# Kernel tuning notes

Hardware: AMD Instinct MI355X
Metric: run time of the kernel (lower is better)

## Reference

```python
import jax, jax.numpy as jnp
import numpy as np

G = 8  # number of shuffle groups (init default)
GN_EPS = 1e-5


def setup_inputs() -> dict:
    key = jax.random.key(0)
    ks = jax.random.split(key, 9)
    C = 512
    cg = C // (2 * G)  # 32: per-branch channel width
    N, H, W = 32, 64, 64
    return {
        "x": jax.random.normal(ks[0], (N, C, H, W), dtype=jnp.float32),
        "cweight": 0.1 * jax.random.normal(ks[1], (1, cg, 1, 1), dtype=jnp.float32),
        "cbias": jnp.ones((1, cg, 1, 1), dtype=jnp.float32),
        "conv1_w": 0.1 * jax.random.normal(ks[2], (cg, cg), dtype=jnp.float32),
        "conv1_b": 0.1 * jax.random.normal(ks[3], (cg,), dtype=jnp.float32),
        "gn_g": jnp.ones((cg,), dtype=jnp.float32),
        "gn_b": jnp.zeros((cg,), dtype=jnp.float32),
        "convh_w": 0.1 * jax.random.normal(ks[4], (cg, cg), dtype=jnp.float32),
        "convh_b": 0.1 * jax.random.normal(ks[5], (cg,), dtype=jnp.float32),
        "convw_w": 0.1 * jax.random.normal(ks[6], (cg, cg), dtype=jnp.float32),
        "convw_b": 0.1 * jax.random.normal(ks[7], (cg,), dtype=jnp.float32),
    }


def _conv1x1(w, b, x):
    # x: [b, ci, h, w] -> [b, co, h, w]
    return jnp.einsum('oi,bihw->bohw', w, x) + b[None, :, None, None]


def _h_swish(y):
    return y * jnp.clip(y + 3.0, 0.0, 6.0) / 6.0


def reference(x, cweight, cbias, conv1_w, conv1_b, gn_g, gn_b,
              convh_w, convh_b, convw_w, convw_b):
    n, c, h, w = x.shape
    xg = x.reshape(n * G, c // G, h, w)          # [nG, 64, h, w]
    x0, x1 = jnp.split(xg, 2, axis=1)            # each [nG, 32, h, w]

    # --- channel attention branch ---
    gap = jnp.mean(x0, axis=(2, 3), keepdims=True)
    x_channel = x0 * jax.nn.sigmoid(cweight * gap + cbias)

    # --- spatial/coordinate attention branch ---
    x_h = jnp.mean(x1, axis=3, keepdims=True)                       # [nG,32,h,1]
    x_w = jnp.mean(x1, axis=2, keepdims=True).transpose(0, 1, 3, 2)  # [nG,32,w,1]
    x_s = jnp.mean(x1, axis=(2, 3), keepdims=True)                  # [nG,32,1,1]

    y = jnp.concatenate([x_h, x_w], axis=2)      # [nG,32,h+w,1]
    y = _conv1x1(conv1_w, conv1_b, y)
    # GroupNorm with groups == channels: per-channel instance norm over spatial dims
    mu = jnp.mean(y, axis=(2, 3), keepdims=True)
    var = jnp.var(y, axis=(2, 3), keepdims=True)
    y = (y - mu) * jax.lax.rsqrt(var + GN_EPS)
    y = y * gn_g[None, :, None, None] + gn_b[None, :, None, None]
    y = _h_swish(y)

    xh, xw = y[:, :, :h, :], y[:, :, h:, :]
    xw = xw.transpose(0, 1, 3, 2)                # [nG,32,1,w]
    a_h = _conv1x1(convh_w, convh_b, xh)         # [nG,32,h,1]
    a_w = _conv1x1(convw_w, convw_b, xw)         # [nG,32,1,w]
    a_hws = a_h * a_w * x_s                      # [nG,32,h,w]
    x_spatial = x1 * jax.nn.sigmoid(a_hws)

    out = jnp.concatenate([x_channel, x_spatial], axis=1)  # [nG,64,h,w]
    out = out.reshape(n, c, h, w)
    # channel shuffle with groups=2
    out = out.reshape(n, 2, c // 2, h, w).transpose(0, 2, 1, 3, 4).reshape(n, c, h, w)
    return out
```

## Files before the change

kernel.cpp:

```cpp
#include <hip/hip_runtime.h>
#include <hip/hip_bf16.h>
#include <math.h>


#define HW 4096
#define CG 32
#define NBG 256

__device__ __forceinline__ float sigmoidf_(float t) {
    return 1.0f / (1.0f + __expf(-t));
}

__global__ __launch_bounds__(256) void k_reduce(
    const float* __restrict__ x,
    const float* __restrict__ cweight, const float* __restrict__ cbias,
    float* __restrict__ out,
    float* __restrict__ x_s, float* __restrict__ x_h, float* __restrict__ x_w) {
    int wid = threadIdx.x >> 6;
    int l   = threadIdx.x & 63;
    int gp  = blockIdx.x * 4 + wid;
    int bg  = gp >> 6;
    int ch  = gp & 63;
    int n = bg >> 3, g = bg & 7;
    const float4* plane = (const float4*)(x + (size_t)(n * 512 + g * 64 + ch) * HW);

    __shared__ float part[4][64][17];

    float4 v[16];
#pragma unroll
    for (int i = 0; i < 16; ++i) v[i] = plane[i * 64 + l];

    float cs0 = 0.f, cs1 = 0.f, cs2 = 0.f, cs3 = 0.f;
#pragma unroll
    for (int i = 0; i < 16; ++i) {
        cs0 += v[i].x; cs1 += v[i].y; cs2 += v[i].z; cs3 += v[i].w;
        part[wid][i * 4 + (l >> 4)][l & 15] = (v[i].x + v[i].y) + (v[i].z + v[i].w);
    }
    cs0 += __shfl_xor(cs0, 16); cs0 += __shfl_xor(cs0, 32);
    cs1 += __shfl_xor(cs1, 16); cs1 += __shfl_xor(cs1, 32);
    cs2 += __shfl_xor(cs2, 16); cs2 += __shfl_xor(cs2, 32);
    cs3 += __shfl_xor(cs3, 16); cs3 += __shfl_xor(cs3, 32);
    float tot = (cs0 + cs1) + (cs2 + cs3);
    tot += __shfl_xor(tot, 1);
    tot += __shfl_xor(tot, 2);
    tot += __shfl_xor(tot, 4);
    tot += __shfl_xor(tot, 8);

    __syncthreads();
    float rsum = 0.f;
#pragma unroll
    for (int j = 0; j < 16; ++j) rsum += part[wid][l][j];

    if (ch < CG) {
        float sc = sigmoidf_(cweight[ch] * (tot * (1.0f / HW)) + cbias[ch]);
        int cc = g * 64 + ch;
        int cf = 2 * (cc & 255) + (cc >> 8);
        float4* dst = (float4*)(out + (size_t)(n * 512 + cf) * HW);
#pragma unroll
        for (int i = 0; i < 16; ++i) {
            float4 t = v[i];
            t.x *= sc; t.y *= sc; t.z *= sc; t.w *= sc;
            dst[i * 64 + l] = t;
        }
    } else {
        int c1 = ch - CG;
        if (l == 0) x_s[bg * CG + c1] = tot * (1.0f / HW);
        x_h[(size_t)(bg * CG + c1) * 64 + l] = rsum * (1.0f / 64.0f);
        if (l < 16) {
            float4 cw;
            cw.x = cs0 * (1.0f / 64.0f); cw.y = cs1 * (1.0f / 64.0f);
            cw.z = cs2 * (1.0f / 64.0f); cw.w = cs3 * (1.0f / 64.0f);
            ((float4*)(x_w + (size_t)(bg * CG + c1) * 64))[l] = cw;
        }
    }
}

__global__ __launch_bounds__(128) void k_mid(
    const float* __restrict__ x_h, const float* __restrict__ x_w,
    const float* __restrict__ x_s,
    const float* __restrict__ w1, const float* __restrict__ b1,
    const float* __restrict__ gn_g, const float* __restrict__ gn_b,
    const float* __restrict__ wh, const float* __restrict__ bh,
    const float* __restrict__ ww, const float* __restrict__ bw,
    float* __restrict__ a_h, float* __restrict__ a_ws) {
    int bg = blockIdx.x;
    int t  = threadIdx.x;

    __shared__ float sy[32][129];
    __shared__ float spart[2][4][32];
    __shared__ float sscale[32], sshift[32];

    float vloc[32];
#pragma unroll
    for (int i = 0; i < 32; ++i) {
        vloc[i] = (t < 64) ? x_h[(size_t)(bg * CG + i) * 64 + t]
                           : x_w[(size_t)(bg * CG + i) * 64 + (t - 64)];
    }

    for (int o = 0; o < 32; ++o) {
        float acc = b1[o];
#pragma unroll
        for (int i = 0; i < 32; ++i) acc += w1[o * 32 + i] * vloc[i];
        sy[o][t] = acc;
    }
    __syncthreads();

    {
        int o = t & 31, seg = t >> 5;
        float s = 0.f, ss = 0.f;
#pragma unroll
        for (int p = 0; p < 32; ++p) {
            float v = sy[o][seg * 32 + p];
            s += v; ss += v * v;
        }
        spart[0][seg][o] = s; spart[1][seg][o] = ss;
    }
    __syncthreads();
    if (t < 32) {
        float s  = spart[0][0][t] + spart[0][1][t] + spart[0][2][t] + spart[0][3][t];
        float ss = spart[1][0][t] + spart[1][1][t] + spart[1][2][t] + spart[1][3][t];
        float mu = s * (1.0f / 128.0f);
        float var = ss * (1.0f / 128.0f) - mu * mu;
        float rstd = rsqrtf(var + 1e-5f);
        float sc = rstd * gn_g[t];
        sscale[t] = sc;
        sshift[t] = gn_b[t] - mu * sc;
    }
    __syncthreads();

    float z[32];
#pragma unroll
    for (int i = 0; i < 32; ++i) {
        float v = sy[i][t] * sscale[i] + sshift[i];
        float c = fminf(fmaxf(v + 3.0f, 0.0f), 6.0f);
        z[i] = v * c * (1.0f / 6.0f);
    }
    if (t < 64) {
        for (int o = 0; o < 32; ++o) {
            float acc = bh[o];
#pragma unroll
            for (int i = 0; i < 32; ++i) acc += wh[o * 32 + i] * z[i];
            a_h[(size_t)(bg * CG + o) * 64 + t] = acc;
        }
    } else {
        int wc = t - 64;
        for (int o = 0; o < 32; ++o) {
            float acc = bw[o];
#pragma unroll
            for (int i = 0; i < 32; ++i) acc += ww[o * 32 + i] * z[i];
            a_ws[(size_t)(bg * CG + o) * 64 + wc] = acc * x_s[bg * CG + o];
        }
    }
}

__global__ __launch_bounds__(256) void k_final(
    const float* __restrict__ x,
    const float* __restrict__ a_h, const float* __restrict__ a_ws,
    float* __restrict__ out) {
    int bid = blockIdx.x;
    int bg = bid >> 5;
    int c1 = bid & 31;
    int n = bg >> 3, g = bg & 7;
    int cc = g * 64 + 32 + c1;
    int cf = 2 * (cc & 255) + (cc >> 8);
    const float4* src = (const float4*)(x   + (size_t)(n * 512 + g * 64 + 32 + c1) * HW);
    float4*       dst = (float4*)      (out + (size_t)(n * 512 + cf) * HW);
    int t = threadIdx.x;

    __shared__ float sah[64], saw[64];
    if (t < 64)       sah[t]      = a_h [(size_t)(bg * CG + c1) * 64 + t];
    else if (t < 128) saw[t - 64] = a_ws[(size_t)(bg * CG + c1) * 64 + (t - 64)];
    __syncthreads();

#pragma unroll
    for (int q = 0; q < 4; ++q) {
        int vi = q * 256 + t;
        float4 v = src[vi];
        int h  = vi >> 4;
        int wb = (vi & 15) * 4;
        float ah = sah[h];
        v.x *= sigmoidf_(ah * saw[wb + 0]);
        v.y *= sigmoidf_(ah * saw[wb + 1]);
        v.z *= sigmoidf_(ah * saw[wb + 2]);
        v.w *= sigmoidf_(ah * saw[wb + 3]);
        dst[vi] = v;
    }
}

extern "C" void kernel_launch(void* const* d_in, const int* in_sizes, int n_in,
                              void* d_out, int out_size, void* d_ws, size_t ws_size,
                              hipStream_t stream) {
    const float* x        = (const float*)d_in[0];
    const float* cweight  = (const float*)d_in[1];
    const float* cbias    = (const float*)d_in[2];
    const float* conv1_w  = (const float*)d_in[3];
    const float* conv1_b  = (const float*)d_in[4];
    const float* gn_g     = (const float*)d_in[5];
    const float* gn_b     = (const float*)d_in[6];
    const float* convh_w  = (const float*)d_in[7];
    const float* convh_b  = (const float*)d_in[8];
    const float* convw_w  = (const float*)d_in[9];
    const float* convw_b  = (const float*)d_in[10];
    float* out = (float*)d_out;

    float* ws   = (float*)d_ws;
    float* x_s  = ws;
    float* x_h  = x_s + NBG * CG;
    float* x_w  = x_h + NBG * CG * 64;
    float* a_h  = x_w + NBG * CG * 64;
    float* a_ws = a_h + NBG * CG * 64;

    k_reduce<<<NBG * 64 / 4, 256, 0, stream>>>(x, cweight, cbias, out, x_s, x_h, x_w);
    k_mid<<<NBG, 128, 0, stream>>>(x_h, x_w, x_s,
                                   conv1_w, conv1_b, gn_g, gn_b,
                                   convh_w, convh_b, convw_w, convw_b,
                                   a_h, a_ws);
    k_final<<<NBG * CG, 256, 0, stream>>>(x, a_h, a_ws, out);
}
```

Measured before the change: 505.8 us.

## Split reduce kernel into channel and pooling kernels, stage weights in LDS

```diff
diff --git a/kernel.cpp b/kernel.cpp
--- a/kernel.cpp
+++ b/kernel.cpp
@@ -1,5 +1,4 @@
 #include <hip/hip_runtime.h>
-#include <hip/hip_bf16.h>
 #include <math.h>
 
 
@@ -7,70 +6,96 @@
 #define CG 32
 #define NBG 256
 
+typedef float f32x4 __attribute__((ext_vector_type(4)));
+
 __device__ __forceinline__ float sigmoidf_(float t) {
     return 1.0f / (1.0f + __expf(-t));
 }
 
-__global__ __launch_bounds__(256) void k_reduce(
+__global__ __launch_bounds__(256) void k_chan(
     const float* __restrict__ x,
     const float* __restrict__ cweight, const float* __restrict__ cbias,
-    float* __restrict__ out,
+    float* __restrict__ out) {
+    int p  = blockIdx.x;
+    int bg = p >> 5, c = p & 31;
+    int n  = bg >> 3, g = bg & 7;
+    const f32x4* src = (const f32x4*)(x + (size_t)(n * 512 + g * 64 + c) * HW);
+    int cc = g * 64 + c;
+    int cf = 2 * (cc & 255) + (cc >> 8);
+    f32x4* dst = (f32x4*)(out + (size_t)(n * 512 + cf) * HW);
+    int t = threadIdx.x;
+
+    f32x4 v[4];
+    float s = 0.f;
+#pragma unroll
+    for (int q = 0; q < 4; ++q) {
+        v[q] = __builtin_nontemporal_load(&src[q * 256 + t]);
+        s += (v[q][0] + v[q][1]) + (v[q][2] + v[q][3]);
+    }
+    s += __shfl_xor(s, 1);  s += __shfl_xor(s, 2);  s += __shfl_xor(s, 4);
+    s += __shfl_xor(s, 8);  s += __shfl_xor(s, 16); s += __shfl_xor(s, 32);
+    __shared__ float wpart[4];
+    if ((t & 63) == 0) wpart[t >> 6] = s;
+    __syncthreads();
+    float tot = (wpart[0] + wpart[1]) + (wpart[2] + wpart[3]);
+    float sc = sigmoidf_(cweight[c] * (tot * (1.0f / HW)) + cbias[c]);
+#pragma unroll
+    for (int q = 0; q < 4; ++q) {
+        f32x4 w = v[q] * sc;
+        __builtin_nontemporal_store(w, &dst[q * 256 + t]);
+    }
+}
+
+__global__ __launch_bounds__(256) void k_pool(
+    const float* __restrict__ x,
     float* __restrict__ x_s, float* __restrict__ x_h, float* __restrict__ x_w) {
-    int wid = threadIdx.x >> 6;
-    int l   = threadIdx.x & 63;
-    int gp  = blockIdx.x * 4 + wid;
-    int bg  = gp >> 6;
-    int ch  = gp & 63;
-    int n = bg >> 3, g = bg & 7;
-    const float4* plane = (const float4*)(x + (size_t)(n * 512 + g * 64 + ch) * HW);
-
-    __shared__ float part[4][64][17];
-
-    float4 v[16];
-#pragma unroll
-    for (int i = 0; i < 16; ++i) v[i] = plane[i * 64 + l];
-
-    float cs0 = 0.f, cs1 = 0.f, cs2 = 0.f, cs3 = 0.f;
-#pragma unroll
-    for (int i = 0; i < 16; ++i) {
-        cs0 += v[i].x; cs1 += v[i].y; cs2 += v[i].z; cs3 += v[i].w;
-        part[wid][i * 4 + (l >> 4)][l & 15] = (v[i].x + v[i].y) + (v[i].z + v[i].w);
-    }
-    cs0 += __shfl_xor(cs0, 16); cs0 += __shfl_xor(cs0, 32);
-    cs1 += __shfl_xor(cs1, 16); cs1 += __shfl_xor(cs1, 32);
-    cs2 += __shfl_xor(cs2, 16); cs2 += __shfl_xor(cs2, 32);
-    cs3 += __shfl_xor(cs3, 16); cs3 += __shfl_xor(cs3, 32);
-    float tot = (cs0 + cs1) + (cs2 + cs3);
-    tot += __shfl_xor(tot, 1);
-    tot += __shfl_xor(tot, 2);
-    tot += __shfl_xor(tot, 4);
-    tot += __shfl_xor(tot, 8);
-
-    __syncthreads();
-    float rsum = 0.f;
-#pragma unroll
-    for (int j = 0; j < 16; ++j) rsum += part[wid][l][j];
-
-    if (ch < CG) {
-        float sc = sigmoidf_(cweight[ch] * (tot * (1.0f / HW)) + cbias[ch]);
-        int cc = g * 64 + ch;
-        int cf = 2 * (cc & 255) + (cc >> 8);
-        float4* dst = (float4*)(out + (size_t)(n * 512 + cf) * HW);
-#pragma unroll
-        for (int i = 0; i < 16; ++i) {
-            float4 t = v[i];
-            t.x *= sc; t.y *= sc; t.z *= sc; t.w *= sc;
-            dst[i * 64 + l] = t;
-        }
-    } else {
-        int c1 = ch - CG;
-        if (l == 0) x_s[bg * CG + c1] = tot * (1.0f / HW);
-        x_h[(size_t)(bg * CG + c1) * 64 + l] = rsum * (1.0f / 64.0f);
-        if (l < 16) {
-            float4 cw;
-            cw.x = cs0 * (1.0f / 64.0f); cw.y = cs1 * (1.0f / 64.0f);
-            cw.z = cs2 * (1.0f / 64.0f); cw.w = cs3 * (1.0f / 64.0f);
-            ((float4*)(x_w + (size_t)(bg * CG + c1) * 64))[l] = cw;
+    int p  = blockIdx.x;
+    int bg = p >> 5, c = p & 31;
+    int n  = bg >> 3, g = bg & 7;
+    const f32x4* src = (const f32x4*)(x + (size_t)(n * 512 + g * 64 + 32 + c) * HW);
+    int t = threadIdx.x;
+    int l = t & 63, wid = t >> 6;
+
+    __shared__ float rowsum[64];
+    __shared__ __align__(16) float colpart[4][64];
+    __shared__ float totpart[4];
+
+    float cx0 = 0.f, cx1 = 0.f, cx2 = 0.f, cx3 = 0.f;
+    float s = 0.f;
+    float rs[4];
+#pragma unroll
+    for (int q = 0; q < 4; ++q) {
+        f32x4 v = src[q * 256 + t];
+        float r4 = (v[0] + v[1]) + (v[2] + v[3]);
+        rs[q] = r4; s += r4;
+        cx0 += v[0]; cx1 += v[1]; cx2 += v[2]; cx3 += v[3];
+    }
+#pragma unroll
+    for (int q = 0; q < 4; ++q) {
+        float r = rs[q];
+        r += __shfl_xor(r, 1); r += __shfl_xor(r, 2);
+        r += __shfl_xor(r, 4); r += __shfl_xor(r, 8);
+        if ((l & 15) == 0) rowsum[q * 16 + (t >> 4)] = r;
+    }
+    cx0 += __shfl_xor(cx0, 16); cx0 += __shfl_xor(cx0, 32);
+    cx1 += __shfl_xor(cx1, 16); cx1 += __shfl_xor(cx1, 32);
+    cx2 += __shfl_xor(cx2, 16); cx2 += __shfl_xor(cx2, 32);
+    cx3 += __shfl_xor(cx3, 16); cx3 += __shfl_xor(cx3, 32);
+    if (l < 16) {
+        f32x4 cw = {cx0, cx1, cx2, cx3};
+        ((f32x4*)&colpart[wid][0])[l] = cw;
+    }
+    s += __shfl_xor(s, 1);  s += __shfl_xor(s, 2);  s += __shfl_xor(s, 4);
+    s += __shfl_xor(s, 8);  s += __shfl_xor(s, 16); s += __shfl_xor(s, 32);
+    if (l == 0) totpart[wid] = s;
+    __syncthreads();
+    if (t < 64) {
+        float cs = (colpart[0][t] + colpart[1][t]) + (colpart[2][t] + colpart[3][t]);
+        x_w[(size_t)(bg * CG + c) * 64 + t] = cs * (1.0f / 64.0f);
+        x_h[(size_t)(bg * CG + c) * 64 + t] = rowsum[t] * (1.0f / 64.0f);
+        if (t == 0) {
+            float tot = (totpart[0] + totpart[1]) + (totpart[2] + totpart[3]);
+            x_s[bg * CG + c] = tot * (1.0f / HW);
         }
     }
 }
@@ -86,21 +111,27 @@
     int bg = blockIdx.x;
     int t  = threadIdx.x;
 
+    __shared__ float sw1[1024], swh[1024], sww[1024];
     __shared__ float sy[32][129];
     __shared__ float spart[2][4][32];
     __shared__ float sscale[32], sshift[32];
 
+    for (int i = t; i < 1024; i += 128) {
+        sw1[i] = w1[i]; swh[i] = wh[i]; sww[i] = ww[i];
+    }
+
     float vloc[32];
 #pragma unroll
     for (int i = 0; i < 32; ++i) {
         vloc[i] = (t < 64) ? x_h[(size_t)(bg * CG + i) * 64 + t]
                            : x_w[(size_t)(bg * CG + i) * 64 + (t - 64)];
     }
+    __syncthreads();
 
     for (int o = 0; o < 32; ++o) {
         float acc = b1[o];
 #pragma unroll
-        for (int i = 0; i < 32; ++i) acc += w1[o * 32 + i] * vloc[i];
+        for (int i = 0; i < 32; ++i) acc += sw1[o * 32 + i] * vloc[i];
         sy[o][t] = acc;
     }
     __syncthreads();
@@ -139,7 +170,7 @@
         for (int o = 0; o < 32; ++o) {
             float acc = bh[o];
 #pragma unroll
-            for (int i = 0; i < 32; ++i) acc += wh[o * 32 + i] * z[i];
+            for (int i = 0; i < 32; ++i) acc += swh[o * 32 + i] * z[i];
             a_h[(size_t)(bg * CG + o) * 64 + t] = acc;
         }
     } else {
@@ -147,7 +178,7 @@
         for (int o = 0; o < 32; ++o) {
             float acc = bw[o];
 #pragma unroll
-            for (int i = 0; i < 32; ++i) acc += ww[o * 32 + i] * z[i];
+            for (int i = 0; i < 32; ++i) acc += sww[o * 32 + i] * z[i];
             a_ws[(size_t)(bg * CG + o) * 64 + wc] = acc * x_s[bg * CG + o];
         }
     }
@@ -163,8 +194,8 @@
     int n = bg >> 3, g = bg & 7;
     int cc = g * 64 + 32 + c1;
     int cf = 2 * (cc & 255) + (cc >> 8);
-    const float4* src = (const float4*)(x   + (size_t)(n * 512 + g * 64 + 32 + c1) * HW);
-    float4*       dst = (float4*)      (out + (size_t)(n * 512 + cf) * HW);
+    const f32x4* src = (const f32x4*)(x   + (size_t)(n * 512 + g * 64 + 32 + c1) * HW);
+    f32x4*       dst = (f32x4*)      (out + (size_t)(n * 512 + cf) * HW);
     int t = threadIdx.x;
 
     __shared__ float sah[64], saw[64];
@@ -175,15 +206,15 @@
 #pragma unroll
     for (int q = 0; q < 4; ++q) {
         int vi = q * 256 + t;
-        float4 v = src[vi];
+        f32x4 v = src[vi];
         int h  = vi >> 4;
         int wb = (vi & 15) * 4;
         float ah = sah[h];
-        v.x *= sigmoidf_(ah * saw[wb + 0]);
-        v.y *= sigmoidf_(ah * saw[wb + 1]);
-        v.z *= sigmoidf_(ah * saw[wb + 2]);
-        v.w *= sigmoidf_(ah * saw[wb + 3]);
-        dst[vi] = v;
+        v[0] *= sigmoidf_(ah * saw[wb + 0]);
+        v[1] *= sigmoidf_(ah * saw[wb + 1]);
+        v[2] *= sigmoidf_(ah * saw[wb + 2]);
+        v[3] *= sigmoidf_(ah * saw[wb + 3]);
+        __builtin_nontemporal_store(v, &dst[vi]);
     }
 }
 
@@ -210,10 +241,11 @@
     float* a_h  = x_w + NBG * CG * 64;
     float* a_ws = a_h + NBG * CG * 64;
 
-    k_reduce<<<NBG * 64 / 4, 256, 0, stream>>>(x, cweight, cbias, out, x_s, x_h, x_w);
-    k_mid<<<NBG, 128, 0, stream>>>(x_h, x_w, x_s,
-                                   conv1_w, conv1_b, gn_g, gn_b,
-                                   convh_w, convh_b, convw_w, convw_b,
-                                   a_h, a_ws);
+    k_chan <<<NBG * CG, 256, 0, stream>>>(x, cweight, cbias, out);
+    k_pool <<<NBG * CG, 256, 0, stream>>>(x, x_s, x_h, x_w);
+    k_mid  <<<NBG, 128, 0, stream>>>(x_h, x_w, x_s,
+                                     conv1_w, conv1_b, gn_g, gn_b,
+                                     convh_w, convh_b, convw_w, convw_b,
+                                     a_h, a_ws);
     k_final<<<NBG * CG, 256, 0, stream>>>(x, a_h, a_ws, out);
 }
```

Result: faster. 481.4 us (-4.8%).
